# Kernel optimization log

Measured on AMD Instinct MI355X. Metric: run time of the kernel, lower is better.

The kernel has to match this reference:

```python
import jax, jax.numpy as jnp
import numpy as np

N, E, IN_DIM, HID = 100000, 1000000, 128, 64


def setup_inputs() -> dict:
    key = jax.random.key(0)
    ks = jax.random.split(key, 9)
    x = jax.random.normal(ks[0], (N, IN_DIM), dtype=jnp.float32)
    edge_index = jax.random.randint(ks[1], (2, E), 0, N, dtype=jnp.int32)
    edge_weight = jax.random.uniform(ks[2], (E,), dtype=jnp.float32)
    # GCNConv / Linear parameters (glorot-ish scaling)
    W1 = jax.random.normal(ks[3], (IN_DIM, HID), dtype=jnp.float32) / np.sqrt(IN_DIM)
    b1 = jnp.zeros((HID,), jnp.float32)
    W2 = jax.random.normal(ks[4], (HID, HID), dtype=jnp.float32) / np.sqrt(HID)
    b2 = jnp.zeros((HID,), jnp.float32)
    Wl = jax.random.normal(ks[5], (HID, 1), dtype=jnp.float32) / np.sqrt(HID)
    bl = jnp.zeros((1,), jnp.float32)
    return {"x": x, "edge_index": edge_index, "edge_weight": edge_weight,
            "W1": W1, "b1": b1, "W2": W2, "b2": b2, "Wl": Wl, "bl": bl}


def _propagate(h, src, dst, norm, num_nodes):
    # gather neighbor features, weight by norm, scatter-add to destinations
    msg = h[src] * norm[:, None]  # [E+N, HID]
    return jax.ops.segment_sum(msg, dst, num_segments=num_nodes)


def reference(x, edge_index, edge_weight, W1, b1, W2, b2, Wl, bl):
    n = x.shape[0]
    loop = jnp.arange(n, dtype=edge_index.dtype)
    # add self-loops with weight 1 (PyG GCNConv default)
    src = jnp.concatenate([edge_index[0], loop])
    dst = jnp.concatenate([edge_index[1], loop])
    ew = jnp.concatenate([edge_weight, jnp.ones((n,), x.dtype)])
    # symmetric normalization: D^-1/2 A D^-1/2
    deg = jax.ops.segment_sum(ew, dst, num_segments=n)
    dinv = jnp.where(deg > 0, jax.lax.rsqrt(deg), 0.0)
    norm = dinv[src] * ew * dinv[dst]  # [E+N]

    h = _propagate(x @ W1, src, dst, norm, n) + b1
    h = jax.nn.relu(h)  # dropout is identity in eval mode
    h = _propagate(h @ W2, src, dst, norm, n) + b2
    h = jax.nn.relu(h)
    return (h @ Wl + bl).squeeze(-1)  # [N]
```

## Files before the change

### kernel.cpp

```cpp
#include <hip/hip_runtime.h>

#define IN_DIM 128
#define HID    64
#define SCAN_B 256
#define NSTRIPE 16

typedef __attribute__((ext_vector_type(4))) _Float16 f16x4;
typedef __attribute__((ext_vector_type(8))) _Float16 f16x8;
typedef __attribute__((ext_vector_type(4))) float    f32x4;

__global__ void k_prep_w(const float* __restrict__ W1, const float* __restrict__ W2,
                         _Float16* __restrict__ W1T, _Float16* __restrict__ W2T) {
    int i = blockIdx.x * blockDim.x + threadIdx.x;
    if (i < IN_DIM * HID) { int k = i >> 6, c = i & 63; W1T[c * IN_DIM + k] = (_Float16)W1[i]; }
    if (i < HID * HID)    { int k = i >> 6, c = i & 63; W2T[c * HID + k]    = (_Float16)W2[i]; }
}

__global__ void k_hist_rank(const int* __restrict__ dst, int* __restrict__ counts_s,
                            int* __restrict__ rank, int n, int e) {
    int i = blockIdx.x * blockDim.x + threadIdx.x;
    if (i < e) {
        int k = (i >> 6) & (NSTRIPE - 1);
        rank[i] = atomicAdd(&counts_s[k * n + dst[i]], 1);
    }
}

__global__ void k_stripe_scan(const int* __restrict__ counts_s, int* __restrict__ P,
                              int* __restrict__ offsets, int n) {
    int v = blockIdx.x * blockDim.x + threadIdx.x;
    if (v >= n) return;
    int acc = 0;
    int pv[NSTRIPE];
    #pragma unroll
    for (int k = 0; k < NSTRIPE; ++k) { pv[k] = acc; acc += counts_s[k * n + v]; }
    #pragma unroll
    for (int k = 0; k < NSTRIPE; ++k) P[v * NSTRIPE + k] = pv[k];
    offsets[v] = acc;
}

__global__ __launch_bounds__(SCAN_B) void k_scan1(int* __restrict__ data,
                                                  int* __restrict__ blockSums, int n) {
    __shared__ int s[SCAN_B];
    int tid = threadIdx.x;
    int gid = blockIdx.x * SCAN_B + tid;
    int v = (gid < n) ? data[gid] : 0;
    s[tid] = v;
    __syncthreads();
    for (int off = 1; off < SCAN_B; off <<= 1) {
        int t = (tid >= off) ? s[tid - off] : 0;
        __syncthreads();
        s[tid] += t;
        __syncthreads();
    }
    if (gid < n) data[gid] = s[tid] - v;
    if (tid == SCAN_B - 1) blockSums[blockIdx.x] = s[tid];
}

__global__ __launch_bounds__(512) void k_scan2(int* __restrict__ blockSums, int nb) {
    __shared__ int s[512];
    int tid = threadIdx.x;
    int v = (tid < nb) ? blockSums[tid] : 0;
    s[tid] = v;
    __syncthreads();
    for (int off = 1; off < 512; off <<= 1) {
        int t = (tid >= off) ? s[tid - off] : 0;
        __syncthreads();
        s[tid] += t;
        __syncthreads();
    }
    if (tid < nb) blockSums[tid] = s[tid] - v;
}

__global__ __launch_bounds__(SCAN_B) void k_scan3_fix(int* __restrict__ data,
                                                      const int* __restrict__ blockSums,
                                                      int* __restrict__ P, int n, int e) {
    int gid = blockIdx.x * SCAN_B + threadIdx.x;
    if (gid < n) {
        int off = data[gid] + blockSums[blockIdx.x];
        data[gid] = off;
        #pragma unroll
        for (int k = 0; k < NSTRIPE; ++k) P[gid * NSTRIPE + k] += off;
        if (gid == n - 1) data[n] = e;
    }
}

__global__ void k_scatter(const int* __restrict__ src, const int* __restrict__ dst,
                          const float* __restrict__ ew, const int* __restrict__ rank,
                          const int* __restrict__ P, int2* __restrict__ sedge, int e) {
    int i = blockIdx.x * blockDim.x + threadIdx.x;
    if (i >= e) return;
    int k = (i >> 6) & (NSTRIPE - 1);
    int pos = P[dst[i] * NSTRIPE + k] + rank[i];
    sedge[pos] = make_int2(src[i], __float_as_int(ew[i]));
}

__global__ void k_deg_dinv(const int* __restrict__ rowOff, const int2* __restrict__ sedge,
                           float* __restrict__ dinv, int n) {
    int v = blockIdx.x * blockDim.x + threadIdx.x;
    if (v >= n) return;
    int s = rowOff[v], t = rowOff[v + 1];
    float a = 1.0f;
    for (int j = s; j < t; ++j) a += __int_as_float(sedge[j].y);
    dinv[v] = rsqrtf(a);
}


__global__ __launch_bounds__(256) void k_gemm1(const float* __restrict__ x,
                                               const _Float16* __restrict__ W1T,
                                               const float* __restrict__ dinv,
                                               _Float16* __restrict__ h0, int n) {
    __shared__ _Float16 sX[4][16 * IN_DIM];
    int tid  = threadIdx.x;
    int wave = tid >> 6, lane = tid & 63;
    int row0 = blockIdx.x * 64 + wave * 16;
    int col  = lane & 15, kg = lane >> 4;

    f16x8 bfrag[4][4];
    #pragma unroll
    for (int ks = 0; ks < 4; ++ks)
        #pragma unroll
        for (int ct = 0; ct < 4; ++ct)
            bfrag[ks][ct] = *(const f16x8*)(W1T + (ct * 16 + col) * IN_DIM + ks * 32 + kg * 8);

    _Float16* myX = sX[wave];
    #pragma unroll
    for (int it = 0; it < 8; ++it) {
        int idx = it * 64 + lane;
        int r = idx >> 5, c4 = idx & 31;
        int grow = row0 + r;
        float4 v = make_float4(0.f, 0.f, 0.f, 0.f);
        if (grow < n) v = ((const float4*)x)[(size_t)grow * 32 + c4];
        f16x4 h; h.x = (_Float16)v.x; h.y = (_Float16)v.y; h.z = (_Float16)v.z; h.w = (_Float16)v.w;
        int off = (r * 256 + c4 * 8) ^ ((r & 7) << 4);
        *(f16x4*)((char*)myX + off) = h;
    }
    __syncthreads();

    f32x4 acc[4];
    #pragma unroll
    for (int ct = 0; ct < 4; ++ct) acc[ct] = (f32x4){0.f, 0.f, 0.f, 0.f};

    int arow = lane & 15;
    #pragma unroll
    for (int ks = 0; ks < 4; ++ks) {
        int off = (arow * 256 + kg * 16 + ks * 64) ^ ((arow & 7) << 4);
        f16x8 af = *(const f16x8*)((const char*)myX + off);
        #pragma unroll
        for (int ct = 0; ct < 4; ++ct)
            acc[ct] = __builtin_amdgcn_mfma_f32_16x16x32_f16(af, bfrag[ks][ct], acc[ct], 0, 0, 0);
    }

    int crow0 = row0 + kg * 4;
    #pragma unroll
    for (int r = 0; r < 4; ++r) {
        int gr = crow0 + r;
        if (gr < n) {
            float dv = dinv[gr];
            #pragma unroll
            for (int ct = 0; ct < 4; ++ct)
                h0[(size_t)gr * HID + ct * 16 + col] = (_Float16)(acc[ct][r] * dv);
        }
    }
}


__global__ __launch_bounds__(256) void k_gemm2(const _Float16* __restrict__ h1,
                                               const _Float16* __restrict__ W2T,
                                               const float* __restrict__ dinv,
                                               _Float16* __restrict__ h2, int n) {
    __shared__ _Float16 sX[4][16 * HID];
    int tid  = threadIdx.x;
    int wave = tid >> 6, lane = tid & 63;
    int row0 = blockIdx.x * 64 + wave * 16;
    int col  = lane & 15, kg = lane >> 4;

    f16x8 bfrag[2][4];
    #pragma unroll
    for (int ks = 0; ks < 2; ++ks)
        #pragma unroll
        for (int ct = 0; ct < 4; ++ct)
            bfrag[ks][ct] = *(const f16x8*)(W2T + (ct * 16 + col) * HID + ks * 32 + kg * 8);

    _Float16* myX = sX[wave];
    #pragma unroll
    for (int it = 0; it < 4; ++it) {
        int idx = it * 64 + lane;
        int r = idx >> 4, c4 = idx & 15;
        int grow = row0 + r;
        f16x4 h = (f16x4){0, 0, 0, 0};
        if (grow < n) h = ((const f16x4*)h1)[(size_t)grow * 16 + c4];
        int off = (r * 128 + c4 * 8) ^ ((r & 7) << 4);
        *(f16x4*)((char*)myX + off) = h;
    }
    __syncthreads();

    f32x4 acc[4];
    #pragma unroll
    for (int ct = 0; ct < 4; ++ct) acc[ct] = (f32x4){0.f, 0.f, 0.f, 0.f};

    int arow = lane & 15;
    #pragma unroll
    for (int ks = 0; ks < 2; ++ks) {
        int off = (arow * 128 + kg * 16 + ks * 64) ^ ((arow & 7) << 4);
        f16x8 af = *(const f16x8*)((const char*)myX + off);
        #pragma unroll
        for (int ct = 0; ct < 4; ++ct)
            acc[ct] = __builtin_amdgcn_mfma_f32_16x16x32_f16(af, bfrag[ks][ct], acc[ct], 0, 0, 0);
    }

    int crow0 = row0 + kg * 4;
    #pragma unroll
    for (int r = 0; r < 4; ++r) {
        int gr = crow0 + r;
        if (gr < n) {
            float dv = dinv[gr];
            #pragma unroll
            for (int ct = 0; ct < 4; ++ct)
                h2[(size_t)gr * HID + ct * 16 + col] = (_Float16)(acc[ct][r] * dv);
        }
    }
}


__global__ __launch_bounds__(256) void k_prop1(const int* __restrict__ rowOff,
                                               const int2* __restrict__ sedge,
                                               const _Float16* __restrict__ hin,
                                               const float* __restrict__ dinv,
                                               const float* __restrict__ b1,
                                               _Float16* __restrict__ hout, int n) {
    int wave = (blockIdx.x * blockDim.x + threadIdx.x) >> 6;
    int lane = threadIdx.x & 63;
    int g    = lane >> 3;
    int gl   = lane & 7;
    int node = wave * 8 + g;
    bool valid = node < n;
    int nd = valid ? node : 0;

    int start = rowOff[nd];
    int end   = valid ? rowOff[nd + 1] : start;
    float di  = dinv[nd];
    float4 bbA = ((const float4*)b1)[gl * 2];
    float4 bbB = ((const float4*)b1)[gl * 2 + 1];

    f16x8 sv = *(const f16x8*)(hin + (size_t)nd * HID + gl * 8);
    float a[8];
    #pragma unroll
    for (int t = 0; t < 8; ++t) a[t] = (float)sv[t];

    int j = start;
    for (; j + 4 <= end; j += 4) {
        int2 e0 = sedge[j], e1 = sedge[j + 1], e2 = sedge[j + 2], e3 = sedge[j + 3];
        f16x8 v0 = *(const f16x8*)(hin + (size_t)e0.x * HID + gl * 8);
        f16x8 v1 = *(const f16x8*)(hin + (size_t)e1.x * HID + gl * 8);
        f16x8 v2 = *(const f16x8*)(hin + (size_t)e2.x * HID + gl * 8);
        f16x8 v3 = *(const f16x8*)(hin + (size_t)e3.x * HID + gl * 8);
        float w0 = __int_as_float(e0.y), w1 = __int_as_float(e1.y);
        float w2 = __int_as_float(e2.y), w3 = __int_as_float(e3.y);
        #pragma unroll
        for (int t = 0; t < 8; ++t) a[t] = fmaf((float)v0[t], w0, a[t]);
        #pragma unroll
        for (int t = 0; t < 8; ++t) a[t] = fmaf((float)v1[t], w1, a[t]);
        #pragma unroll
        for (int t = 0; t < 8; ++t) a[t] = fmaf((float)v2[t], w2, a[t]);
        #pragma unroll
        for (int t = 0; t < 8; ++t) a[t] = fmaf((float)v3[t], w3, a[t]);
    }
    if (j < end) {
        #pragma unroll
        for (int k = 0; k < 4; ++k) {
            int idx = j + k;
            int cl  = idx < end ? idx : j;
            int2 ed = sedge[cl];
            float w = idx < end ? __int_as_float(ed.y) : 0.0f;
            f16x8 v = *(const f16x8*)(hin + (size_t)ed.x * HID + gl * 8);
            #pragma unroll
            for (int t = 0; t < 8; ++t) a[t] = fmaf((float)v[t], w, a[t]);
        }
    }

    if (valid) {
        f16x8 o;
        o[0] = (_Float16)fmaxf(fmaf(a[0], di, bbA.x), 0.0f);
        o[1] = (_Float16)fmaxf(fmaf(a[1], di, bbA.y), 0.0f);
        o[2] = (_Float16)fmaxf(fmaf(a[2], di, bbA.z), 0.0f);
        o[3] = (_Float16)fmaxf(fmaf(a[3], di, bbA.w), 0.0f);
        o[4] = (_Float16)fmaxf(fmaf(a[4], di, bbB.x), 0.0f);
        o[5] = (_Float16)fmaxf(fmaf(a[5], di, bbB.y), 0.0f);
        o[6] = (_Float16)fmaxf(fmaf(a[6], di, bbB.z), 0.0f);
        o[7] = (_Float16)fmaxf(fmaf(a[7], di, bbB.w), 0.0f);
        *(f16x8*)(hout + (size_t)node * HID + gl * 8) = o;
    }
}

__global__ __launch_bounds__(256) void k_prop2_final(const int* __restrict__ rowOff,
                                                     const int2* __restrict__ sedge,
                                                     const _Float16* __restrict__ hin,
                                                     const float* __restrict__ dinv,
                                                     const float* __restrict__ b2,
                                                     const float* __restrict__ Wl,
                                                     const float* __restrict__ bl,
                                                     float* __restrict__ out, int n) {
    int wave = (blockIdx.x * blockDim.x + threadIdx.x) >> 6;
    int lane = threadIdx.x & 63;
    int g    = lane >> 3;
    int gl   = lane & 7;
    int node = wave * 8 + g;
    bool valid = node < n;
    int nd = valid ? node : 0;

    int start = rowOff[nd];
    int end   = valid ? rowOff[nd + 1] : start;
    float di  = dinv[nd];
    float4 bbA = ((const float4*)b2)[gl * 2];
    float4 bbB = ((const float4*)b2)[gl * 2 + 1];
    float4 wlA = ((const float4*)Wl)[gl * 2];
    float4 wlB = ((const float4*)Wl)[gl * 2 + 1];

    f16x8 sv = *(const f16x8*)(hin + (size_t)nd * HID + gl * 8);
    float a[8];
    #pragma unroll
    for (int t = 0; t < 8; ++t) a[t] = (float)sv[t];

    int j = start;
    for (; j + 4 <= end; j += 4) {
        int2 e0 = sedge[j], e1 = sedge[j + 1], e2 = sedge[j + 2], e3 = sedge[j + 3];
        f16x8 v0 = *(const f16x8*)(hin + (size_t)e0.x * HID + gl * 8);
        f16x8 v1 = *(const f16x8*)(hin + (size_t)e1.x * HID + gl * 8);
        f16x8 v2 = *(const f16x8*)(hin + (size_t)e2.x * HID + gl * 8);
        f16x8 v3 = *(const f16x8*)(hin + (size_t)e3.x * HID + gl * 8);
        float w0 = __int_as_float(e0.y), w1 = __int_as_float(e1.y);
        float w2 = __int_as_float(e2.y), w3 = __int_as_float(e3.y);
        #pragma unroll
        for (int t = 0; t < 8; ++t) a[t] = fmaf((float)v0[t], w0, a[t]);
        #pragma unroll
        for (int t = 0; t < 8; ++t) a[t] = fmaf((float)v1[t], w1, a[t]);
        #pragma unroll
        for (int t = 0; t < 8; ++t) a[t] = fmaf((float)v2[t], w2, a[t]);
        #pragma unroll
        for (int t = 0; t < 8; ++t) a[t] = fmaf((float)v3[t], w3, a[t]);
    }
    if (j < end) {
        #pragma unroll
        for (int k = 0; k < 4; ++k) {
            int idx = j + k;
            int cl  = idx < end ? idx : j;
            int2 ed = sedge[cl];
            float w = idx < end ? __int_as_float(ed.y) : 0.0f;
            f16x8 v = *(const f16x8*)(hin + (size_t)ed.x * HID + gl * 8);
            #pragma unroll
            for (int t = 0; t < 8; ++t) a[t] = fmaf((float)v[t], w, a[t]);
        }
    }

    float bb[8] = {bbA.x, bbA.y, bbA.z, bbA.w, bbB.x, bbB.y, bbB.z, bbB.w};
    float wl[8] = {wlA.x, wlA.y, wlA.z, wlA.w, wlB.x, wlB.y, wlB.z, wlB.w};
    float v = 0.0f;
    #pragma unroll
    for (int t = 0; t < 8; ++t)
        v += fmaxf(fmaf(a[t], di, bb[t]), 0.0f) * wl[t];
    #pragma unroll
    for (int off = 1; off < 8; off <<= 1)
        v += __shfl_xor(v, off);
    if (valid && gl == 0) out[node] = v + bl[0];
}


static inline char* align16(char* p) {
    return (char*)(((uintptr_t)p + 15) & ~(uintptr_t)15);
}

extern "C" void kernel_launch(void* const* d_in, const int* in_sizes, int n_in,
                              void* d_out, int out_size, void* d_ws, size_t ws_size,
                              hipStream_t stream) {
    const float* x   = (const float*)d_in[0];
    const int*   ei  = (const int*)d_in[1];
    const float* ew  = (const float*)d_in[2];
    const float* W1  = (const float*)d_in[3];
    const float* b1  = (const float*)d_in[4];
    const float* W2  = (const float*)d_in[5];
    const float* b2  = (const float*)d_in[6];
    const float* Wl  = (const float*)d_in[7];
    const float* bl  = (const float*)d_in[8];

    const int n = in_sizes[0] / IN_DIM;
    const int e = in_sizes[2];
    const int* src = ei;
    const int* dst = ei + e;

    float* out = (float*)d_out;
    const int B256 = 256;
    const int nScanBlocks = (n + SCAN_B - 1) / SCAN_B;

    char* p = (char*)d_ws;
    int2*     sedge    = (int2*)p;            p += (size_t)e * 8;
    float*    dinv     = (float*)p;           p += (size_t)n * 4;
    int*      offsets  = (int*)p;             p += ((size_t)n + 1) * 4;
    p = align16(p);
    int*      bsums    = (int*)p;             p += 512 * 4;
    int*      rank     = (int*)p;             p += (size_t)e * 4;
    p = align16(p);
    int*      counts_s = (int*)p;             p += (size_t)NSTRIPE * n * 4;
    int*      P        = (int*)p;             p += (size_t)NSTRIPE * n * 4;
    _Float16* W1T      = (_Float16*)p;        p += IN_DIM * HID * 2;
    _Float16* W2T      = (_Float16*)p;        p += HID * HID * 2;
    p = align16(p);
    _Float16* A        = (_Float16*)p;        p += (size_t)n * HID * 2;
    _Float16* B        = (_Float16*)p;        p += (size_t)n * HID * 2;

    k_prep_w<<<(IN_DIM * HID + B256 - 1) / B256, B256, 0, stream>>>(W1, W2, W1T, W2T);

    hipMemsetAsync(counts_s, 0, (size_t)NSTRIPE * n * 4, stream);

    k_hist_rank<<<(e + B256 - 1) / B256, B256, 0, stream>>>(dst, counts_s, rank, n, e);

    k_stripe_scan<<<(n + B256 - 1) / B256, B256, 0, stream>>>(counts_s, P, offsets, n);

    k_scan1<<<nScanBlocks, SCAN_B, 0, stream>>>(offsets, bsums, n);
    k_scan2<<<1, 512, 0, stream>>>(bsums, nScanBlocks);
    k_scan3_fix<<<nScanBlocks, SCAN_B, 0, stream>>>(offsets, bsums, P, n, e);

    k_scatter<<<(e + B256 - 1) / B256, B256, 0, stream>>>(src, dst, ew, rank, P, sedge, e);

    k_deg_dinv<<<(n + B256 - 1) / B256, B256, 0, stream>>>(offsets, sedge, dinv, n);

    const int gemmBlocks = (n + 63) / 64;
    const int propBlocks = (n + 31) / 32;

    k_gemm1<<<gemmBlocks, B256, 0, stream>>>(x, W1T, dinv, A, n);
    k_prop1<<<propBlocks, B256, 0, stream>>>(offsets, sedge, A, dinv, b1, B, n);

    k_gemm2<<<gemmBlocks, B256, 0, stream>>>(B, W2T, dinv, A, n);
    k_prop2_final<<<propBlocks, B256, 0, stream>>>(offsets, sedge, A, dinv,
                                                   b2, Wl, bl, out, n);
}
```

Measured before the change: 207.7 us.

## Replace global-atomic striped histogram with LDS-binned chunk histograms for CSR build

Builds the destination-sorted edge list by splitting edges into chunks of 16384 and nodes into ranges of 16384. Each block counts its range in shared-memory atomics and writes 16-bit per-chunk histograms. A column scan then turns these into per-chunk prefixes, which removes the global atomics, the memset and the striped prefix array P. The cost is that every block rereads its chunk of dst once per node range (about 7x redundant reads), plus a serial scan over about 62 chunks per node. The 16-bit counts assume no chunk holds more than 65535 edges for one node.

```diff
diff --git a/kernel.cpp b/kernel.cpp
--- a/kernel.cpp
+++ b/kernel.cpp
@@ -3,7 +3,10 @@
 #define IN_DIM 128
 #define HID    64
 #define SCAN_B 256
-#define NSTRIPE 16
+#define RSIZE  16384
+#define CSHIFT 14
+#define CSIZE  (1 << CSHIFT)
+#define NCMAX  64
 
 typedef __attribute__((ext_vector_type(4))) _Float16 f16x4;
 typedef __attribute__((ext_vector_type(8))) _Float16 f16x8;
@@ -16,26 +19,47 @@
     if (i < HID * HID)    { int k = i >> 6, c = i & 63; W2T[c * HID + k]    = (_Float16)W2[i]; }
 }
 
-__global__ void k_hist_rank(const int* __restrict__ dst, int* __restrict__ counts_s,
-                            int* __restrict__ rank, int n, int e) {
-    int i = blockIdx.x * blockDim.x + threadIdx.x;
-    if (i < e) {
-        int k = (i >> 6) & (NSTRIPE - 1);
-        rank[i] = atomicAdd(&counts_s[k * n + dst[i]], 1);
-    }
-}
-
-__global__ void k_stripe_scan(const int* __restrict__ counts_s, int* __restrict__ P,
-                              int* __restrict__ offsets, int n) {
+__global__ __launch_bounds__(256) void k_bin_hist(const int* __restrict__ dst,
+                                                  unsigned short* __restrict__ hist16,
+                                                  int* __restrict__ rank,
+                                                  int n, int e) {
+    __shared__ int cnt[RSIZE];
+    int c = blockIdx.x, r = blockIdx.y;
+    int tid = threadIdx.x;
+    int4* c4 = (int4*)cnt;
+    #pragma unroll
+    for (int k = 0; k < RSIZE / 4 / 256; ++k) c4[tid + k * 256] = make_int4(0, 0, 0, 0);
+    __syncthreads();
+
+    int base = r * RSIZE;
+    int i0 = c << CSHIFT;
+    int i1 = min(e, i0 + CSIZE);
+    for (int i = i0 + tid; i < i1; i += 256) {
+        int d = dst[i];
+        unsigned rel = (unsigned)(d - base);
+        if (rel < RSIZE) rank[i] = atomicAdd(&cnt[rel], 1);
+    }
+    __syncthreads();
+
+    size_t hb = (size_t)c * n;
+    for (int j = tid; j < RSIZE; j += 256) {
+        int v = base + j;
+        if (v < n) hist16[hb + v] = (unsigned short)cnt[j];
+    }
+}
+
+__global__ void k_chunk_scan(unsigned short* __restrict__ hist16,
+                             int* __restrict__ offsets, int n, int nc) {
     int v = blockIdx.x * blockDim.x + threadIdx.x;
     if (v >= n) return;
-    int acc = 0;
-    int pv[NSTRIPE];
-    #pragma unroll
-    for (int k = 0; k < NSTRIPE; ++k) { pv[k] = acc; acc += counts_s[k * n + v]; }
-    #pragma unroll
-    for (int k = 0; k < NSTRIPE; ++k) P[v * NSTRIPE + k] = pv[k];
-    offsets[v] = acc;
+    int run = 0;
+    for (int c = 0; c < nc; ++c) {
+        size_t idx = (size_t)c * n + v;
+        int t = hist16[idx];
+        hist16[idx] = (unsigned short)run;
+        run += t;
+    }
+    offsets[v] = run;
 }
 
 __global__ __launch_bounds__(SCAN_B) void k_scan1(int* __restrict__ data,
@@ -71,26 +95,26 @@
     if (tid < nb) blockSums[tid] = s[tid] - v;
 }
 
-__global__ __launch_bounds__(SCAN_B) void k_scan3_fix(int* __restrict__ data,
-                                                      const int* __restrict__ blockSums,
-                                                      int* __restrict__ P, int n, int e) {
+__global__ __launch_bounds__(SCAN_B) void k_scan3(int* __restrict__ data,
+                                                  const int* __restrict__ blockSums,
+                                                  int n, int e) {
     int gid = blockIdx.x * SCAN_B + threadIdx.x;
     if (gid < n) {
-        int off = data[gid] + blockSums[blockIdx.x];
-        data[gid] = off;
-        #pragma unroll
-        for (int k = 0; k < NSTRIPE; ++k) P[gid * NSTRIPE + k] += off;
+        data[gid] += blockSums[blockIdx.x];
         if (gid == n - 1) data[n] = e;
     }
 }
 
 __global__ void k_scatter(const int* __restrict__ src, const int* __restrict__ dst,
                           const float* __restrict__ ew, const int* __restrict__ rank,
-                          const int* __restrict__ P, int2* __restrict__ sedge, int e) {
+                          const int* __restrict__ offsets,
+                          const unsigned short* __restrict__ hist16,
+                          int2* __restrict__ sedge, int n, int e) {
     int i = blockIdx.x * blockDim.x + threadIdx.x;
     if (i >= e) return;
-    int k = (i >> 6) & (NSTRIPE - 1);
-    int pos = P[dst[i] * NSTRIPE + k] + rank[i];
+    int d = dst[i];
+    int c = i >> CSHIFT;
+    int pos = offsets[d] + (int)hist16[(size_t)c * n + d] + rank[i];
     sedge[pos] = make_int2(src[i], __float_as_int(ew[i]));
 }
 
@@ -390,36 +414,37 @@
     float* out = (float*)d_out;
     const int B256 = 256;
     const int nScanBlocks = (n + SCAN_B - 1) / SCAN_B;
+    const int nc = (e + CSIZE - 1) >> CSHIFT;
+    const int nr = (n + RSIZE - 1) / RSIZE;
 
     char* p = (char*)d_ws;
-    int2*     sedge    = (int2*)p;            p += (size_t)e * 8;
-    float*    dinv     = (float*)p;           p += (size_t)n * 4;
-    int*      offsets  = (int*)p;             p += ((size_t)n + 1) * 4;
+    int2*           sedge   = (int2*)p;            p += (size_t)e * 8;
+    float*          dinv    = (float*)p;           p += (size_t)n * 4;
+    int*            offsets = (int*)p;             p += ((size_t)n + 1) * 4;
     p = align16(p);
-    int*      bsums    = (int*)p;             p += 512 * 4;
-    int*      rank     = (int*)p;             p += (size_t)e * 4;
+    int*            bsums   = (int*)p;             p += 512 * 4;
+    int*            rank    = (int*)p;             p += (size_t)e * 4;
     p = align16(p);
-    int*      counts_s = (int*)p;             p += (size_t)NSTRIPE * n * 4;
-    int*      P        = (int*)p;             p += (size_t)NSTRIPE * n * 4;
-    _Float16* W1T      = (_Float16*)p;        p += IN_DIM * HID * 2;
-    _Float16* W2T      = (_Float16*)p;        p += HID * HID * 2;
+    unsigned short* hist16  = (unsigned short*)p;  p += (size_t)NCMAX * n * 2;
+    _Float16*       W1T     = (_Float16*)p;        p += IN_DIM * HID * 2;
+    _Float16*       W2T     = (_Float16*)p;        p += HID * HID * 2;
     p = align16(p);
-    _Float16* A        = (_Float16*)p;        p += (size_t)n * HID * 2;
-    _Float16* B        = (_Float16*)p;        p += (size_t)n * HID * 2;
+    _Float16*       A       = (_Float16*)p;        p += (size_t)n * HID * 2;
+    _Float16*       B       = (_Float16*)p;        p += (size_t)n * HID * 2;
 
     k_prep_w<<<(IN_DIM * HID + B256 - 1) / B256, B256, 0, stream>>>(W1, W2, W1T, W2T);
 
-    hipMemsetAsync(counts_s, 0, (size_t)NSTRIPE * n * 4, stream);
-
-    k_hist_rank<<<(e + B256 - 1) / B256, B256, 0, stream>>>(dst, counts_s, rank, n, e);
-
-    k_stripe_scan<<<(n + B256 - 1) / B256, B256, 0, stream>>>(counts_s, P, offsets, n);
+    dim3 binGrid(nc, nr);
+    k_bin_hist<<<binGrid, B256, 0, stream>>>(dst, hist16, rank, n, e);
+
+    k_chunk_scan<<<(n + B256 - 1) / B256, B256, 0, stream>>>(hist16, offsets, n, nc);
 
     k_scan1<<<nScanBlocks, SCAN_B, 0, stream>>>(offsets, bsums, n);
     k_scan2<<<1, 512, 0, stream>>>(bsums, nScanBlocks);
-    k_scan3_fix<<<nScanBlocks, SCAN_B, 0, stream>>>(offsets, bsums, P, n, e);
-
-    k_scatter<<<(e + B256 - 1) / B256, B256, 0, stream>>>(src, dst, ew, rank, P, sedge, e);
+    k_scan3<<<nScanBlocks, SCAN_B, 0, stream>>>(offsets, bsums, n, e);
+
+    k_scatter<<<(e + B256 - 1) / B256, B256, 0, stream>>>(src, dst, ew, rank,
+                                                         offsets, hist16, sedge, n, e);
 
     k_deg_dinv<<<(n + B256 - 1) / B256, B256, 0, stream>>>(offsets, sedge, dinv, n);
 
```

After: 199.9 us. -3.8%, faster.
